# Performance work log

Hardware: AMD Instinct MI355X
Metric: run time of the kernel (lower is better)

## Reference

```python
import jax, jax.numpy as jnp
import numpy as np


def setup_inputs() -> dict:
    key = jax.random.key(0)
    k1, k2, k3 = jax.random.split(key, 3)
    B, C, H, W = 32, 2048, 14, 14
    OUT = 512
    x = jax.random.normal(k1, (B, C, H, W), dtype=jnp.float32)
    gamma = jnp.zeros((1,), dtype=jnp.float32)  # nn.Parameter(torch.zeros(1))
    # 1x1 conv 2048 -> 512 (layer=4 branch), kaiming-ish scale
    conv_w = jax.random.normal(k2, (OUT, C, 1, 1), dtype=jnp.float32) * (1.0 / np.sqrt(C))
    conv_b = jax.random.normal(k3, (OUT,), dtype=jnp.float32) * 0.01
    return {"x": x, "gamma": gamma, "conv_w": conv_w, "conv_b": conv_b}


def reference(x, gamma, conv_w, conv_b):
    B, C, H, W = x.shape
    q = x.reshape(B, C, H * W)                      # [B, C, N]
    # energy[b, c, d] = <q[b,c,:], q[b,d,:]>
    energy = jnp.einsum('bcn,bdn->bcd', q, q)       # [B, C, C]
    # max-subtract trick: softmax(max - energy) along last dim
    energy_new = jnp.max(energy, axis=-1, keepdims=True) - energy
    attention = jax.nn.softmax(energy_new, axis=-1)  # [B, C, C]
    out = jnp.einsum('bcd,bdn->bcn', attention, q).reshape(B, C, H, W)
    out = gamma * out + x
    # 1x1 conv, stride 1, no padding (layer=4 branch)
    pam_out = jax.lax.conv_general_dilated(
        out, conv_w, window_strides=(1, 1), padding='VALID',
        dimension_numbers=('NCHW', 'OIHW', 'NCHW'))
    pam_out = pam_out + conv_b[None, :, None, None]
    return pam_out
```

## Files before the change

kernel.cpp:

```cpp
#include <hip/hip_runtime.h>
#include <hip/hip_bf16.h>
#include <stdint.h>

#define B_   32
#define C_   2048
#define HW_  196
#define OUT_ 512
#define KT_  128
#define NKT  (C_ / KT_)
#define BN_  112
#define LDSS 132

typedef short short8 __attribute__((ext_vector_type(8)));
typedef float floatx4 __attribute__((ext_vector_type(4)));
typedef unsigned short u16;

__device__ __forceinline__ uint32_t pack_bf16(float a, float b) {
  union { __hip_bfloat162 h; uint32_t u; } c;
  c.h = __float22bfloat162_rn(make_float2(a, b));
  return c.u;
}

#define BAR_SYNC() asm volatile("s_waitcnt lgkmcnt(0)\n\ts_barrier" ::: "memory")

__global__ void prep_kernel(const float* __restrict__ w, u16* __restrict__ wbf,
                            const float* __restrict__ x,
                            const float* __restrict__ gamma,
                            float* __restrict__ y) {
  if (blockIdx.x < 1024) {
    int gid = blockIdx.x * 256 + threadIdx.x;
    float4 v = ((const float4*)w)[gid];
    ((uint2*)wbf)[gid] = make_uint2(pack_bf16(v.x, v.y), pack_bf16(v.z, v.w));
    return;
  }
  float gm = gamma[0];
  if (gm == 0.0f || y == nullptr) return;
  __shared__ float qc[HW_];
  __shared__ float e[C_];
  __shared__ float red[256];
  int tid = threadIdx.x;
  for (int cRow = (int)blockIdx.x - 1024; cRow < C_; cRow += 256) {
    for (int b = 0; b < B_; ++b) {
      const float* q = x + (size_t)b * C_ * HW_;
      __syncthreads();
      for (int i = tid; i < HW_; i += 256) qc[i] = q[(size_t)cRow * HW_ + i];
      __syncthreads();
      for (int d = tid; d < C_; d += 256) {
        float s = 0.f;
        const float* qd = q + (size_t)d * HW_;
        for (int n = 0; n < HW_; ++n) s += qc[n] * qd[n];
        e[d] = s;
      }
      __syncthreads();
      float mn = 3.4e38f;
      for (int d = tid; d < C_; d += 256) mn = fminf(mn, e[d]);
      red[tid] = mn; __syncthreads();
      for (int s2 = 128; s2 > 0; s2 >>= 1) { if (tid < s2) red[tid] = fminf(red[tid], red[tid + s2]); __syncthreads(); }
      float emin = red[0];
      __syncthreads();
      float ps = 0.f;
      for (int d = tid; d < C_; d += 256) { float p = __expf(emin - e[d]); e[d] = p; ps += p; }
      red[tid] = ps; __syncthreads();
      for (int s2 = 128; s2 > 0; s2 >>= 1) { if (tid < s2) red[tid] += red[tid + s2]; __syncthreads(); }
      float S = red[0];
      __syncthreads();
      float invS = 1.f / S;
      for (int n = tid; n < HW_; n += 256) {
        float acc2 = 0.f;
        for (int d = 0; d < C_; ++d) acc2 += e[d] * q[(size_t)d * HW_ + n];
        y[((size_t)b * C_ + cRow) * HW_ + n] = gm * acc2 * invS + q[(size_t)cRow * HW_ + n];
      }
    }
  }
}

__global__ __launch_bounds__(256, 1) void conv_gemm(
    const float* __restrict__ x, const float* __restrict__ yws,
    const float* __restrict__ gamma, const u16* __restrict__ wbf,
    const float* __restrict__ bias, float* __restrict__ out, int have_y) {

  __shared__ __align__(16) u16 Bs[2][BN_ * LDSS];

  const int tid  = threadIdx.x;
  const int wave = tid >> 6;
  const int lane = tid & 63;
  const int col  = lane & 15;
  const int quad = lane >> 4;

  const int bid  = blockIdx.x;
  const int xcd  = bid & 7;
  const int s    = bid >> 3;
  const int ot   = s & 3;
  const int gset = s >> 2;
  const int g    = gset * 8 + xcd;
  const int b    = g >> 1;
  const int nh   = g & 1;
  const int n0   = nh * (HW_ - BN_);
  const int oBase= ot * 128;

  const float* src = (have_y && gamma[0] != 0.0f) ? yws : x;
  const float* panel = src + (size_t)b * C_ * HW_ + n0;

  int gOff[7], lOff[7];
#pragma unroll
  for (int i = 0; i < 7; ++i) {
    int idx = i * 256 + tid;
    int u = idx / 56;
    int v = idx - u * 56;
    gOff[i] = u * 4 * HW_ + 2 * v;
    lOff[i] = (2 * v) * LDSS + 4 * u;
  }

  int rowOff[7];
#pragma unroll
  for (int nt = 0; nt < 7; ++nt) rowOff[nt] = (nt * 16 + col) * LDSS + quad * 8;

  const u16* aRow = wbf + (size_t)(oBase + wave * 32 + col) * C_ + quad * 8;

  floatx4 acc[2][7];
#pragma unroll
  for (int m = 0; m < 2; ++m)
#pragma unroll
    for (int nt = 0; nt < 7; ++nt) { floatx4 z = {0.f, 0.f, 0.f, 0.f}; acc[m][nt] = z; }

  float2 sv[7][4];
  uint4  aR[8];

  auto stageLoad = [&](int kt) {
    const float* p = panel + (size_t)kt * KT_ * HW_;
#pragma unroll
    for (int i = 0; i < 7; ++i) {
      const float* q = p + gOff[i];
#pragma unroll
      for (int r = 0; r < 4; ++r) sv[i][r] = *(const float2*)(q + r * HW_);
    }
  };
  auto loadA = [&](int kt) {
#pragma unroll
    for (int m = 0; m < 2; ++m)
#pragma unroll
      for (int ks = 0; ks < 4; ++ks)
        aR[m * 4 + ks] = *(const uint4*)(aRow + (size_t)m * 16 * C_ + kt * KT_ + ks * 32);
  };
  auto stageWrite = [&](u16* bb) {
#pragma unroll
    for (int i = 0; i < 7; ++i) {
      uint2 w0 = make_uint2(pack_bf16(sv[i][0].x, sv[i][1].x),
                            pack_bf16(sv[i][2].x, sv[i][3].x));
      uint2 w1 = make_uint2(pack_bf16(sv[i][0].y, sv[i][1].y),
                            pack_bf16(sv[i][2].y, sv[i][3].y));
      *(uint2*)(bb + lOff[i])        = w0;
      *(uint2*)(bb + lOff[i] + LDSS) = w1;
    }
  };
  auto phase = [&](const u16* bb) {
#pragma unroll
    for (int ks = 0; ks < 4; ++ks) {
      union { uint4 u; short8 v; } a0, a1;
      a0.u = aR[ks]; a1.u = aR[4 + ks];
#pragma unroll
      for (int nt = 0; nt < 7; ++nt) {
        const u16* fp = bb + rowOff[nt] + ks * 32;
        union { uint2 p[2]; short8 v; } bf;
        bf.p[0] = *(const uint2*)fp;
        bf.p[1] = *(const uint2*)(fp + 4);
        acc[0][nt] = __builtin_amdgcn_mfma_f32_16x16x32_bf16(a0.v, bf.v, acc[0][nt], 0, 0, 0);
        acc[1][nt] = __builtin_amdgcn_mfma_f32_16x16x32_bf16(a1.v, bf.v, acc[1][nt], 0, 0, 0);
      }
    }
  };

  stageLoad(0);
  loadA(0);
  stageWrite(Bs[0]);
  stageLoad(1);
  BAR_SYNC();

  u16* cur = Bs[0]; u16* nxt = Bs[1];
  for (int kt = 0; kt < NKT; ++kt) {
    phase(cur);
    if (kt + 1 < NKT) {
      loadA(kt + 1);
      stageWrite(nxt);
      if (kt + 2 < NKT) stageLoad(kt + 2);
      BAR_SYNC();
      u16* t = cur; cur = nxt; nxt = t;
    }
  }

  float* outb = out + (size_t)b * OUT_ * HW_ + n0;
#pragma unroll
  for (int m = 0; m < 2; ++m)
#pragma unroll
    for (int r = 0; r < 4; ++r) {
      int o = oBase + wave * 32 + m * 16 + quad * 4 + r;
      float bv = bias[o];
      float* orow = outb + (size_t)o * HW_;
#pragma unroll
      for (int nt = 0; nt < 7; ++nt)
        orow[nt * 16 + col] = acc[m][nt][r] + bv;
    }
}

extern "C" void kernel_launch(void* const* d_in, const int* in_sizes, int n_in,
                              void* d_out, int out_size, void* d_ws, size_t ws_size,
                              hipStream_t stream) {
  const float* x      = (const float*)d_in[0];
  const float* gamma  = (const float*)d_in[1];
  const float* conv_w = (const float*)d_in[2];
  const float* conv_b = (const float*)d_in[3];
  float* out = (float*)d_out;

  const size_t wbf_bytes = (size_t)OUT_ * C_ * sizeof(u16);
  const size_t y_bytes   = (size_t)B_ * C_ * HW_ * sizeof(float);
  u16*   wbf = (u16*)d_ws;
  float* yws = (float*)((char*)d_ws + wbf_bytes);
  int have_y = ws_size >= wbf_bytes + y_bytes;

  int prep_grid = have_y ? 1280 : 1024;
  prep_kernel<<<dim3(prep_grid), dim3(256), 0, stream>>>(
      conv_w, wbf, x, gamma, have_y ? yws : nullptr);
  conv_gemm<<<dim3(256), dim3(256), 0, stream>>>(
      x, have_y ? yws : x, gamma, wbf, conv_b, out, have_y);
}
```

Baseline: 130.1 us.

## Split GEMM N-tile to 64 columns, double grid, prefetch A two stages ahead

Shrinks the spatial tile from 112 to 64 columns (four overlapping tiles per batch covering 196), doubling the grid to 512 blocks and allowing two blocks per CU. The A-operand registers are double-buffered and the k-loop is unrolled by two, so weight loads for k+2 are issued while the current stage computes. This aims to raise occupancy and latency hiding across 256 CUs. In exchange it recomputes the overlapping 60 columns and reloads the weights for each extra tile.

```diff
diff --git a/kernel.cpp b/kernel.cpp
--- a/kernel.cpp
+++ b/kernel.cpp
@@ -8,7 +8,8 @@
 #define OUT_ 512
 #define KT_  128
 #define NKT  (C_ / KT_)
-#define BN_  112
+#define BN_  64
+#define NTI  4
 #define LDSS 132
 
 typedef short short8 __attribute__((ext_vector_type(8)));
@@ -74,7 +75,7 @@
   }
 }
 
-__global__ __launch_bounds__(256, 1) void conv_gemm(
+__global__ __launch_bounds__(256, 2) void conv_gemm(
     const float* __restrict__ x, const float* __restrict__ yws,
     const float* __restrict__ gamma, const u16* __restrict__ wbf,
     const float* __restrict__ bias, float* __restrict__ out, int have_y) {
@@ -91,51 +92,51 @@
   const int xcd  = bid & 7;
   const int s    = bid >> 3;
   const int ot   = s & 3;
-  const int gset = s >> 2;
-  const int g    = gset * 8 + xcd;
-  const int b    = g >> 1;
-  const int nh   = g & 1;
-  const int n0   = nh * (HW_ - BN_);
+  const int gl   = s >> 2;
+  const int grp  = xcd * 16 + gl;
+  const int b    = grp >> 2;
+  const int n0i  = grp & 3;
+  const int n0   = (n0i < 3) ? n0i * 64 : (HW_ - BN_);
   const int oBase= ot * 128;
 
   const float* src = (have_y && gamma[0] != 0.0f) ? yws : x;
   const float* panel = src + (size_t)b * C_ * HW_ + n0;
 
-  int gOff[7], lOff[7];
-#pragma unroll
-  for (int i = 0; i < 7; ++i) {
+  int gOff[4], lOff[4];
+#pragma unroll
+  for (int i = 0; i < 4; ++i) {
     int idx = i * 256 + tid;
-    int u = idx / 56;
-    int v = idx - u * 56;
+    int u = idx >> 5;
+    int v = idx & 31;
     gOff[i] = u * 4 * HW_ + 2 * v;
     lOff[i] = (2 * v) * LDSS + 4 * u;
   }
 
-  int rowOff[7];
-#pragma unroll
-  for (int nt = 0; nt < 7; ++nt) rowOff[nt] = (nt * 16 + col) * LDSS + quad * 8;
+  int rowOff[NTI];
+#pragma unroll
+  for (int nt = 0; nt < NTI; ++nt) rowOff[nt] = (nt * 16 + col) * LDSS + quad * 8;
 
   const u16* aRow = wbf + (size_t)(oBase + wave * 32 + col) * C_ + quad * 8;
 
-  floatx4 acc[2][7];
+  floatx4 acc[2][NTI];
 #pragma unroll
   for (int m = 0; m < 2; ++m)
 #pragma unroll
-    for (int nt = 0; nt < 7; ++nt) { floatx4 z = {0.f, 0.f, 0.f, 0.f}; acc[m][nt] = z; }
-
-  float2 sv[7][4];
-  uint4  aR[8];
+    for (int nt = 0; nt < NTI; ++nt) { floatx4 z = {0.f, 0.f, 0.f, 0.f}; acc[m][nt] = z; }
+
+  float2 sv[4][4];
+  uint4  aR0[8], aR1[8];
 
   auto stageLoad = [&](int kt) {
     const float* p = panel + (size_t)kt * KT_ * HW_;
 #pragma unroll
-    for (int i = 0; i < 7; ++i) {
+    for (int i = 0; i < 4; ++i) {
       const float* q = p + gOff[i];
 #pragma unroll
       for (int r = 0; r < 4; ++r) sv[i][r] = *(const float2*)(q + r * HW_);
     }
   };
-  auto loadA = [&](int kt) {
+  auto loadA = [&](int kt, uint4* aR) {
 #pragma unroll
     for (int m = 0; m < 2; ++m)
 #pragma unroll
@@ -144,7 +145,7 @@
   };
   auto stageWrite = [&](u16* bb) {
 #pragma unroll
-    for (int i = 0; i < 7; ++i) {
+    for (int i = 0; i < 4; ++i) {
       uint2 w0 = make_uint2(pack_bf16(sv[i][0].x, sv[i][1].x),
                             pack_bf16(sv[i][2].x, sv[i][3].x));
       uint2 w1 = make_uint2(pack_bf16(sv[i][0].y, sv[i][1].y),
@@ -153,13 +154,13 @@
       *(uint2*)(bb + lOff[i] + LDSS) = w1;
     }
   };
-  auto phase = [&](const u16* bb) {
+  auto phase = [&](const u16* bb, const uint4* aR) {
 #pragma unroll
     for (int ks = 0; ks < 4; ++ks) {
       union { uint4 u; short8 v; } a0, a1;
       a0.u = aR[ks]; a1.u = aR[4 + ks];
 #pragma unroll
-      for (int nt = 0; nt < 7; ++nt) {
+      for (int nt = 0; nt < NTI; ++nt) {
         const u16* fp = bb + rowOff[nt] + ks * 32;
         union { uint2 p[2]; short8 v; } bf;
         bf.p[0] = *(const uint2*)fp;
@@ -171,20 +172,23 @@
   };
 
   stageLoad(0);
-  loadA(0);
+  loadA(0, aR0);
   stageWrite(Bs[0]);
   stageLoad(1);
+  loadA(1, aR1);
   BAR_SYNC();
 
-  u16* cur = Bs[0]; u16* nxt = Bs[1];
-  for (int kt = 0; kt < NKT; ++kt) {
-    phase(cur);
-    if (kt + 1 < NKT) {
-      loadA(kt + 1);
-      stageWrite(nxt);
-      if (kt + 2 < NKT) stageLoad(kt + 2);
+  for (int k2 = 0; k2 < NKT / 2; ++k2) {
+    const int kt = k2 * 2;
+    phase(Bs[0], aR0);
+    stageWrite(Bs[1]);
+    if (kt + 2 < NKT) { stageLoad(kt + 2); loadA(kt + 2, aR0); }
+    BAR_SYNC();
+    phase(Bs[1], aR1);
+    if (kt + 2 < NKT) {
+      stageWrite(Bs[0]);
+      if (kt + 3 < NKT) { stageLoad(kt + 3); loadA(kt + 3, aR1); }
       BAR_SYNC();
-      u16* t = cur; cur = nxt; nxt = t;
     }
   }
 
@@ -197,7 +201,7 @@
       float bv = bias[o];
       float* orow = outb + (size_t)o * HW_;
 #pragma unroll
-      for (int nt = 0; nt < 7; ++nt)
+      for (int nt = 0; nt < NTI; ++nt)
         orow[nt * 16 + col] = acc[m][nt][r] + bv;
     }
 }
@@ -220,6 +224,6 @@
   int prep_grid = have_y ? 1280 : 1024;
   prep_kernel<<<dim3(prep_grid), dim3(256), 0, stream>>>(
       conv_w, wbf, x, gamma, have_y ? yws : nullptr);
-  conv_gemm<<<dim3(256), dim3(256), 0, stream>>>(
+  conv_gemm<<<dim3(512), dim3(256), 0, stream>>>(
       x, have_y ? yws : x, gamma, wbf, conv_b, out, have_y);
 }
```

After: 137.3 us. 1.05x slower.
